# Kernel optimization log

Measured on AMD Instinct MI355X. Metric: run time of the kernel, lower is better.

The kernel has to match this reference:

```python
import jax, jax.numpy as jnp
import numpy as np

B, N, F, FH, H = 8, 2048, 64, 64, 4
NEG_BIG = -1e10


def setup_inputs() -> dict:
    key = jax.random.key(0)
    k_x, k_a, k_w, k_as, k_an = jax.random.split(key, 5)
    X = jax.random.normal(k_x, (B, N, F), dtype=jnp.float32)
    A = (jax.random.uniform(k_a, (B, N, N)) < 0.1).astype(jnp.float32)
    A = jnp.maximum(A, jnp.eye(N, dtype=jnp.float32)[None])
    W = jax.random.normal(k_w, (H, F, FH), dtype=jnp.float32) * (1.0 / np.sqrt(F))
    b = jnp.zeros((H, FH), dtype=jnp.float32)
    a_self = jax.random.normal(k_as, (H, FH), dtype=jnp.float32) * (1.0 / np.sqrt(FH))
    a_neigh = jax.random.normal(k_an, (H, FH), dtype=jnp.float32) * (1.0 / np.sqrt(FH))
    return {"X": X, "A": A, "W": W, "b": b, "a_self": a_self, "a_neigh": a_neigh}


def reference(X, A, W, b, a_self, a_neigh):
    # per-head linear projection: [B,H,N,FH]
    feats = jnp.einsum("bnf,hfo->bhno", X, W)
    # additive attention logits: e_ij = leaky_relu(a_s.h_i + a_n.h_j)
    s_self = jnp.einsum("bhno,ho->bhn", feats, a_self)   # [B,H,N]
    s_neigh = jnp.einsum("bhno,ho->bhn", feats, a_neigh)  # [B,H,N]
    scores = s_self[:, :, :, None] + s_neigh[:, :, None, :]  # [B,H,N,N]
    scores = jax.nn.leaky_relu(scores, negative_slope=0.2)
    scores = scores + (1.0 - A)[:, None] * NEG_BIG  # adjacency mask
    attn = jax.nn.softmax(scores, axis=-1)
    # weighted aggregation + bias (dropouts are identity at inference)
    out = jnp.einsum("bhnm,bhmo->bhno", attn, feats) + b[None, :, None, :]
    # concat heads -> [B,N,H*FH], then activation
    Bd, Hd, Nd, Fd = out.shape
    out = jnp.transpose(out, (0, 2, 1, 3)).reshape(Bd, Nd, Hd * Fd)
    return jax.nn.relu(out)
```

## Files before the change

kernel.cpp:

```cpp
#include <hip/hip_runtime.h>
#include <hip/hip_bf16.h>
#include <stdint.h>

#define B_ 8
#define N_ 2048
#define F_ 64
#define FH_ 64
#define H_ 4
#define C_ (H_*FH_)
#define CHUNK 64
#define NCHUNK (N_/CHUNK)
#define LOG2E 1.44269504088896340736f

typedef short short8 __attribute__((ext_vector_type(8)));
typedef float f32x4 __attribute__((ext_vector_type(4)));

__device__ __forceinline__ short f2bf(float f) {
    __hip_bfloat16 h = __float2bfloat16(f);
    return __builtin_bit_cast(short, h);
}

__device__ __forceinline__ void async16(void* l, const void* g) {
    __builtin_amdgcn_global_load_lds((const __attribute__((address_space(1))) unsigned int*)g,
                                     (__attribute__((address_space(3))) unsigned int*)l, 16, 0, 0);
}

__global__ __launch_bounds__(256) void kf(const float* __restrict__ A,
                                          const float* __restrict__ X,
                                          const float* __restrict__ W,
                                          const float* __restrict__ a_self,
                                          const float* __restrict__ a_neigh,
                                          unsigned long long* __restrict__ Amask,
                                          __hip_bfloat16* __restrict__ featsT,
                                          float* __restrict__ ss,
                                          float* __restrict__ sn) {
    __shared__ float a_lds[2][FH_];
    __shared__ __hip_bfloat16 cw_lds[FH_ * 72];
    const int bx = blockIdx.x;
    const int tid = threadIdx.x;
    const int wave = tid >> 6, lane = tid & 63;

    if (bx >= 1024) {
        const int R = (bx - 1024) * 4 + wave;
        const float* arow = A + (size_t)R * N_;
        unsigned long long* mrow = Amask + (size_t)R * (N_ / 64);
#pragma unroll
        for (int i = 0; i < 8; ++i) {
            float a0 = arow[i * 256 + lane];
            float a1 = arow[i * 256 + 64 + lane];
            float a2 = arow[i * 256 + 128 + lane];
            float a3 = arow[i * 256 + 192 + lane];
            unsigned long long m0 = __ballot(a0 != 0.0f);
            unsigned long long m1 = __ballot(a1 != 0.0f);
            unsigned long long m2 = __ballot(a2 != 0.0f);
            unsigned long long m3 = __ballot(a3 != 0.0f);
            if (lane == 0) {
                mrow[i * 4 + 0] = m0; mrow[i * 4 + 1] = m1;
                mrow[i * 4 + 2] = m2; mrow[i * 4 + 3] = m3;
            }
        }
        return;
    }

    const int nb = bx & 31, h = (bx >> 5) & 3, b = bx >> 7;

    if (tid < 64)       a_lds[0][tid] = a_self[h * FH_ + tid];
    else if (tid < 128) a_lds[1][tid - 64] = a_neigh[h * FH_ + tid - 64];
    {
        int f = tid >> 2, o0 = (tid & 3) * 16;
        const float* wsrc = W + ((size_t)(h * F_ + f)) * FH_ + o0;
#pragma unroll
        for (int k = 0; k < 16; ++k)
            cw_lds[(o0 + k) * 72 + f] = __float2bfloat16(wsrc[k]);
    }
    __syncthreads();

    const int m = lane & 15, q = lane >> 4;
    const int nl = wave * 16 + m;
    const int n = nb * 64 + nl;
    f32x4 acc[4] = {};
#pragma unroll
    for (int ks = 0; ks < 2; ++ks) {
        const float* xp = X + ((size_t)(b * N_ + n)) * F_ + ks * 32 + q * 8;
        float4 x0 = *(const float4*)xp;
        float4 x1 = *(const float4*)(xp + 4);
        short8 bfrag;
        bfrag[0] = f2bf(x0.x); bfrag[1] = f2bf(x0.y);
        bfrag[2] = f2bf(x0.z); bfrag[3] = f2bf(x0.w);
        bfrag[4] = f2bf(x1.x); bfrag[5] = f2bf(x1.y);
        bfrag[6] = f2bf(x1.z); bfrag[7] = f2bf(x1.w);
#pragma unroll
        for (int ot = 0; ot < 4; ++ot) {
            short8 afrag = *(const short8*)(cw_lds + (ot * 16 + m) * 72 + ks * 32 + q * 8);
            acc[ot] = __builtin_amdgcn_mfma_f32_16x16x32_bf16(afrag, bfrag, acc[ot], 0, 0, 0);
        }
    }
    __syncthreads();
    float ssv = 0.f, snv = 0.f;
#pragma unroll
    for (int ot = 0; ot < 4; ++ot) {
#pragma unroll
        for (int r = 0; r < 4; ++r) {
            int orow = ot * 16 + q * 4 + r;
            float v = acc[ot][r];
            cw_lds[orow * 72 + nl] = __float2bfloat16(v);
            ssv += v * a_lds[0][orow];
            snv += v * a_lds[1][orow];
        }
    }
    ssv += __shfl_xor(ssv, 16); ssv += __shfl_xor(ssv, 32);
    snv += __shfl_xor(snv, 16); snv += __shfl_xor(snv, 32);
    __syncthreads();
    {
        int o = tid >> 2, c = (tid & 3) * 16;
        const __hip_bfloat16* src = cw_lds + o * 72 + c;
        __hip_bfloat16* dst = featsT + ((size_t)(b * H_ + h) * FH_ + o) * N_ + nb * 64 + c;
        *(uint4*)dst       = *(const uint4*)src;
        *(uint4*)(dst + 8) = *(const uint4*)(src + 8);
    }
    if (lane < 16) {
        size_t idx = ((size_t)(b * H_ + h)) * N_ + n;
        ss[idx] = ssv * LOG2E;
        sn[idx] = snv * LOG2E;
    }
}

__global__ __launch_bounds__(256, 4) void k3_attn(const unsigned int* __restrict__ Amask,
                                                  const __hip_bfloat16* __restrict__ featsT,
                                                  const float* __restrict__ ss,
                                                  const float* __restrict__ sn,
                                                  const float* __restrict__ bias,
                                                  float* __restrict__ out) {
    __shared__ __hip_bfloat16 fv_lds[2][64 * CHUNK];
    __shared__ float e1_lds[N_];
    __shared__ float e2_lds[N_];

    const int L = blockIdx.x;
    const int g = L & 7;
    const int s = L >> 3;
    const int bh = g * 4 + (s >> 5);
    const int tile = s & 31;
    const int b = bh >> 2, h = bh & 3;

    const int tid = threadIdx.x, wave = tid >> 6, lane = tid & 63;
    const int m = lane & 15, q = lane >> 4;
    const int rowtile = tile * 64;

    {
        const float4* snrow = (const float4*)(sn + ((size_t)(b * H_ + h)) * N_);
        float4* e1v = (float4*)e1_lds;
        float4* e2v = (float4*)e2_lds;
#pragma unroll
        for (int i = 0; i < 2; ++i) {
            int idx = tid + i * 256;
            float4 v = snrow[idx];
            float4 u1, u2;
            u1.x = exp2f(v.x); u1.y = exp2f(v.y); u1.z = exp2f(v.z); u1.w = exp2f(v.w);
            u2.x = exp2f(0.2f * v.x); u2.y = exp2f(0.2f * v.y);
            u2.z = exp2f(0.2f * v.z); u2.w = exp2f(0.2f * v.w);
            e1v[idx] = u1; e2v[idx] = u2;
        }
    }
    const float ssi = ss[((size_t)(b * H_ + h)) * N_ + rowtile + wave * 16 + m];
    const float e1i = exp2f(ssi), e2i = exp2f(0.2f * ssi);

    const __hip_bfloat16* fhead = featsT + ((size_t)(b * H_ + h)) * FH_ * N_;
    const unsigned int* mrow = Amask + ((size_t)(b * N_) + rowtile + wave * 16 + m) * (N_ / 32);

    auto stage = [&](int c, int bufi) {
        const int cb = c * CHUNK;
#pragma unroll
        for (int i = 0; i < 2; ++i) {
            int base_unit = i * 256 + wave * 64;
            int unit = base_unit + lane;
            int o = unit >> 3, v = unit & 7;
            int u = v ^ (o & 7);
            async16(&fv_lds[bufi][base_unit * 8], fhead + (size_t)o * N_ + cb + u * 8);
        }
    };

    auto buildP = [&](int c, unsigned int mA, unsigned int mB, short8& pA, short8& pB) {
        const int cg = c * CHUNK;
        float4 eA10 = *(const float4*)(e1_lds + cg + q * 8);
        float4 eA11 = *(const float4*)(e1_lds + cg + q * 8 + 4);
        float4 eB10 = *(const float4*)(e1_lds + cg + 32 + q * 8);
        float4 eB11 = *(const float4*)(e1_lds + cg + 32 + q * 8 + 4);
        float4 eA20 = *(const float4*)(e2_lds + cg + q * 8);
        float4 eA21 = *(const float4*)(e2_lds + cg + q * 8 + 4);
        float4 eB20 = *(const float4*)(e2_lds + cg + 32 + q * 8);
        float4 eB21 = *(const float4*)(e2_lds + cg + 32 + q * 8 + 4);
        float e1A[8] = {eA10.x, eA10.y, eA10.z, eA10.w, eA11.x, eA11.y, eA11.z, eA11.w};
        float e1B[8] = {eB10.x, eB10.y, eB10.z, eB10.w, eB11.x, eB11.y, eB11.z, eB11.w};
        float e2A[8] = {eA20.x, eA20.y, eA20.z, eA20.w, eA21.x, eA21.y, eA21.z, eA21.w};
        float e2B[8] = {eB20.x, eB20.y, eB20.z, eB20.w, eB21.x, eB21.y, eB21.z, eB21.w};
#pragma unroll
        for (int t = 0; t < 8; ++t) {
            float vA = fmaxf(e1i * e1A[t], e2i * e2A[t]);
            float vB = fmaxf(e1i * e1B[t], e2i * e2B[t]);
            const int bit = q * 8 + t;
            pA[t] = (mA >> bit) & 1 ? f2bf(vA) : (short)0;
            pB[t] = (mB >> bit) & 1 ? f2bf(vB) : (short)0;
        }
    };

    uint2 mk_use = *(const uint2*)(mrow + 0);
    uint2 mk_a   = *(const uint2*)(mrow + 2);

    stage(0, 0);
    __syncthreads();

    f32x4 acc[2][4] = {};
    f32x4 accl[2] = {};
    short8 ones;
#pragma unroll
    for (int t = 0; t < 8; ++t) ones[t] = (short)0x3F80;

    short8 pA, pB;
    buildP(0, mk_use.x, mk_use.y, pA, pB);

    for (int c = 0; c < NCHUNK; ++c) {
        const int cur = c & 1;
        if (c + 1 < NCHUNK) stage(c + 1, cur ^ 1);
        uint2 mk_b = mk_a;
        if (c + 2 < NCHUNK) mk_b = *(const uint2*)(mrow + (c + 2) * 2);

        short8 fA[4], fB[4];
#pragma unroll
        for (int ct = 0; ct < 4; ++ct) {
            int o = ct * 16 + m;
            fA[ct] = *(const short8*)(fv_lds[cur] + ((o << 3) + (q ^ (o & 7))) * 8);
            fB[ct] = *(const short8*)(fv_lds[cur] + ((o << 3) + ((4 + q) ^ (o & 7))) * 8);
        }
#pragma unroll
        for (int ct = 0; ct < 4; ++ct) {
            acc[0][ct] = __builtin_amdgcn_mfma_f32_16x16x32_bf16(pA, fA[ct], acc[0][ct], 0, 0, 0);
            acc[1][ct] = __builtin_amdgcn_mfma_f32_16x16x32_bf16(pB, fB[ct], acc[1][ct], 0, 0, 0);
        }
        accl[0] = __builtin_amdgcn_mfma_f32_16x16x32_bf16(pA, ones, accl[0], 0, 0, 0);
        accl[1] = __builtin_amdgcn_mfma_f32_16x16x32_bf16(pB, ones, accl[1], 0, 0, 0);

        if (c + 1 < NCHUNK) buildP(c + 1, mk_a.x, mk_a.y, pA, pB);
        mk_a = mk_b;

        __syncthreads();
    }

    float bc[4];
#pragma unroll
    for (int ct = 0; ct < 4; ++ct) bc[ct] = bias[h * FH_ + ct * 16 + m];

#pragma unroll
    for (int r = 0; r < 4; ++r) {
        float inv = 1.0f / (accl[0][r] + accl[1][r]);
        int gr = rowtile + wave * 16 + q * 4 + r;
#pragma unroll
        for (int ct = 0; ct < 4; ++ct) {
            float v = (acc[0][ct][r] + acc[1][ct][r]) * inv + bc[ct];
            out[((size_t)(b * N_) + gr) * C_ + h * FH_ + ct * 16 + m] = fmaxf(v, 0.0f);
        }
    }
}

extern "C" void kernel_launch(void* const* d_in, const int* in_sizes, int n_in,
                              void* d_out, int out_size, void* d_ws, size_t ws_size,
                              hipStream_t stream) {
    const float* X       = (const float*)d_in[0];
    const float* A       = (const float*)d_in[1];
    const float* W       = (const float*)d_in[2];
    const float* bias    = (const float*)d_in[3];
    const float* a_self  = (const float*)d_in[4];
    const float* a_neigh = (const float*)d_in[5];
    float* out = (float*)d_out;

    char* ws = (char*)d_ws;
    __hip_bfloat16* featsT = (__hip_bfloat16*)(ws);
    float* ss              = (float*)(ws + 8421376);
    float* sn              = (float*)(ws + 8683520);
    unsigned long long* Am = (unsigned long long*)(ws + 8945664);

    kf      <<<5120, 256, 0, stream>>>(A, X, W, a_self, a_neigh, Am, featsT, ss, sn);
    k3_attn <<<1024, 256, 0, stream>>>((const unsigned int*)Am, featsT, ss, sn, bias, out);
}
```

Before: 250.4 us.

## Split attention columns across waves with per-wave staging and cross-wave reduction

Each wave now covers all 64 rows of the tile but only its own 512-column slice of neighbours. It stages its own feature chunk into a private LDS buffer, which removes the block-wide __syncthreads in the main loop and replaces them with per-wave waitcnt fences. Partial accumulators and row sums are combined through an LDS tree reduction at the end. The cost is more registers (launch bounds lowered from 4 to 2 blocks), reduction overhead, and an extra stall where each wave waits on its own async load with no double buffering.

```diff
diff --git a/kernel.cpp b/kernel.cpp
--- a/kernel.cpp
+++ b/kernel.cpp
@@ -9,7 +9,6 @@
 #define H_ 4
 #define C_ (H_*FH_)
 #define CHUNK 64
-#define NCHUNK (N_/CHUNK)
 #define LOG2E 1.44269504088896340736f
 
 typedef short short8 __attribute__((ext_vector_type(8)));
@@ -125,26 +124,24 @@
     }
 }
 
-__global__ __launch_bounds__(256, 4) void k3_attn(const unsigned int* __restrict__ Amask,
+__global__ __launch_bounds__(256, 2) void k3_attn(const unsigned int* __restrict__ Amask,
                                                   const __hip_bfloat16* __restrict__ featsT,
                                                   const float* __restrict__ ss,
                                                   const float* __restrict__ sn,
                                                   const float* __restrict__ bias,
                                                   float* __restrict__ out) {
-    __shared__ __hip_bfloat16 fv_lds[2][64 * CHUNK];
-    __shared__ float e1_lds[N_];
-    __shared__ float e2_lds[N_];
-
-    const int L = blockIdx.x;
-    const int g = L & 7;
-    const int s = L >> 3;
-    const int bh = g * 4 + (s >> 5);
-    const int tile = s & 31;
-    const int b = bh >> 2, h = bh & 3;
-
+    __shared__ char smem[49152];
+    float* e1_lds = (float*)smem;
+    float* e2_lds = (float*)(smem + 8192);
+    __hip_bfloat16* fv_all = (__hip_bfloat16*)(smem + 16384);
+
+    const int bx = blockIdx.x;
+    const int tile = bx & 31, h = (bx >> 5) & 3, b = bx >> 7;
     const int tid = threadIdx.x, wave = tid >> 6, lane = tid & 63;
     const int m = lane & 15, q = lane >> 4;
     const int rowtile = tile * 64;
+    const int colbase = wave * 512;
+    __hip_bfloat16* fvw = fv_all + wave * 4096;
 
     {
         const float4* snrow = (const float4*)(sn + ((size_t)(b * H_ + h)) * N_);
@@ -161,102 +158,152 @@
             e1v[idx] = u1; e2v[idx] = u2;
         }
     }
-    const float ssi = ss[((size_t)(b * H_ + h)) * N_ + rowtile + wave * 16 + m];
-    const float e1i = exp2f(ssi), e2i = exp2f(0.2f * ssi);
+    const float* ssrow = ss + ((size_t)(b * H_ + h)) * N_ + rowtile;
+    float e1i[4], e2i[4];
+#pragma unroll
+    for (int rg = 0; rg < 4; ++rg) {
+        float s_ = ssrow[rg * 16 + m];
+        e1i[rg] = exp2f(s_); e2i[rg] = exp2f(0.2f * s_);
+    }
 
     const __hip_bfloat16* fhead = featsT + ((size_t)(b * H_ + h)) * FH_ * N_;
-    const unsigned int* mrow = Amask + ((size_t)(b * N_) + rowtile + wave * 16 + m) * (N_ / 32);
-
-    auto stage = [&](int c, int bufi) {
-        const int cb = c * CHUNK;
-#pragma unroll
-        for (int i = 0; i < 2; ++i) {
-            int base_unit = i * 256 + wave * 64;
-            int unit = base_unit + lane;
+    const unsigned int* mrow = Amask + ((size_t)(b * N_) + rowtile + m) * (N_ / 32) + (colbase >> 5);
+
+    auto stage = [&](int c) {
+        const int cb = colbase + c * CHUNK;
+#pragma unroll
+        for (int i = 0; i < 8; ++i) {
+            int unit = i * 64 + lane;
             int o = unit >> 3, v = unit & 7;
             int u = v ^ (o & 7);
-            async16(&fv_lds[bufi][base_unit * 8], fhead + (size_t)o * N_ + cb + u * 8);
+            async16(fvw + (size_t)(i * 64) * 8, fhead + (size_t)o * N_ + cb + u * 8);
         }
     };
 
-    auto buildP = [&](int c, unsigned int mA, unsigned int mB, short8& pA, short8& pB) {
-        const int cg = c * CHUNK;
-        float4 eA10 = *(const float4*)(e1_lds + cg + q * 8);
-        float4 eA11 = *(const float4*)(e1_lds + cg + q * 8 + 4);
-        float4 eB10 = *(const float4*)(e1_lds + cg + 32 + q * 8);
-        float4 eB11 = *(const float4*)(e1_lds + cg + 32 + q * 8 + 4);
-        float4 eA20 = *(const float4*)(e2_lds + cg + q * 8);
-        float4 eA21 = *(const float4*)(e2_lds + cg + q * 8 + 4);
-        float4 eB20 = *(const float4*)(e2_lds + cg + 32 + q * 8);
-        float4 eB21 = *(const float4*)(e2_lds + cg + 32 + q * 8 + 4);
-        float e1A[8] = {eA10.x, eA10.y, eA10.z, eA10.w, eA11.x, eA11.y, eA11.z, eA11.w};
-        float e1B[8] = {eB10.x, eB10.y, eB10.z, eB10.w, eB11.x, eB11.y, eB11.z, eB11.w};
-        float e2A[8] = {eA20.x, eA20.y, eA20.z, eA20.w, eA21.x, eA21.y, eA21.z, eA21.w};
-        float e2B[8] = {eB20.x, eB20.y, eB20.z, eB20.w, eB21.x, eB21.y, eB21.z, eB21.w};
-#pragma unroll
-        for (int t = 0; t < 8; ++t) {
-            float vA = fmaxf(e1i * e1A[t], e2i * e2A[t]);
-            float vB = fmaxf(e1i * e1B[t], e2i * e2B[t]);
-            const int bit = q * 8 + t;
-            pA[t] = (mA >> bit) & 1 ? f2bf(vA) : (short)0;
-            pB[t] = (mB >> bit) & 1 ? f2bf(vB) : (short)0;
-        }
-    };
-
-    uint2 mk_use = *(const uint2*)(mrow + 0);
-    uint2 mk_a   = *(const uint2*)(mrow + 2);
-
-    stage(0, 0);
-    __syncthreads();
-
-    f32x4 acc[2][4] = {};
-    f32x4 accl[2] = {};
+    uint2 mk[4];
+#pragma unroll
+    for (int rg = 0; rg < 4; ++rg) mk[rg] = *(const uint2*)(mrow + rg * 1024);
+    stage(0);
+    __syncthreads();
+
+    f32x4 acc[4][4] = {};
+    f32x4 accl[4] = {};
     short8 ones;
 #pragma unroll
     for (int t = 0; t < 8; ++t) ones[t] = (short)0x3F80;
 
-    short8 pA, pB;
-    buildP(0, mk_use.x, mk_use.y, pA, pB);
-
-    for (int c = 0; c < NCHUNK; ++c) {
-        const int cur = c & 1;
-        if (c + 1 < NCHUNK) stage(c + 1, cur ^ 1);
-        uint2 mk_b = mk_a;
-        if (c + 2 < NCHUNK) mk_b = *(const uint2*)(mrow + (c + 2) * 2);
-
+    for (int c = 0; c < 8; ++c) {
         short8 fA[4], fB[4];
 #pragma unroll
         for (int ct = 0; ct < 4; ++ct) {
             int o = ct * 16 + m;
-            fA[ct] = *(const short8*)(fv_lds[cur] + ((o << 3) + (q ^ (o & 7))) * 8);
-            fB[ct] = *(const short8*)(fv_lds[cur] + ((o << 3) + ((4 + q) ^ (o & 7))) * 8);
-        }
-#pragma unroll
-        for (int ct = 0; ct < 4; ++ct) {
-            acc[0][ct] = __builtin_amdgcn_mfma_f32_16x16x32_bf16(pA, fA[ct], acc[0][ct], 0, 0, 0);
-            acc[1][ct] = __builtin_amdgcn_mfma_f32_16x16x32_bf16(pB, fB[ct], acc[1][ct], 0, 0, 0);
-        }
-        accl[0] = __builtin_amdgcn_mfma_f32_16x16x32_bf16(pA, ones, accl[0], 0, 0, 0);
-        accl[1] = __builtin_amdgcn_mfma_f32_16x16x32_bf16(pB, ones, accl[1], 0, 0, 0);
-
-        if (c + 1 < NCHUNK) buildP(c + 1, mk_a.x, mk_a.y, pA, pB);
-        mk_a = mk_b;
-
-        __syncthreads();
-    }
-
-    float bc[4];
-#pragma unroll
-    for (int ct = 0; ct < 4; ++ct) bc[ct] = bias[h * FH_ + ct * 16 + m];
-
-#pragma unroll
-    for (int r = 0; r < 4; ++r) {
-        float inv = 1.0f / (accl[0][r] + accl[1][r]);
-        int gr = rowtile + wave * 16 + q * 4 + r;
-#pragma unroll
-        for (int ct = 0; ct < 4; ++ct) {
-            float v = (acc[0][ct][r] + acc[1][ct][r]) * inv + bc[ct];
-            out[((size_t)(b * N_) + gr) * C_ + h * FH_ + ct * 16 + m] = fmaxf(v, 0.0f);
+            fA[ct] = *(const short8*)(fvw + ((o << 3) + (q ^ (o & 7))) * 8);
+            fB[ct] = *(const short8*)(fvw + ((o << 3) + ((4 + q) ^ (o & 7))) * 8);
+        }
+        asm volatile("s_waitcnt lgkmcnt(0)" ::: "memory");
+        __builtin_amdgcn_sched_barrier(0);
+        if (c + 1 < 8) stage(c + 1);
+        uint2 mkn[4];
+        if (c + 1 < 8) {
+#pragma unroll
+            for (int rg = 0; rg < 4; ++rg) mkn[rg] = *(const uint2*)(mrow + rg * 1024 + (c + 1) * 2);
+        }
+
+        const int cb = colbase + c * CHUNK;
+        float4 a10 = *(const float4*)(e1_lds + cb + q * 8);
+        float4 a11 = *(const float4*)(e1_lds + cb + q * 8 + 4);
+        float4 b10 = *(const float4*)(e1_lds + cb + 32 + q * 8);
+        float4 b11 = *(const float4*)(e1_lds + cb + 32 + q * 8 + 4);
+        float4 a20 = *(const float4*)(e2_lds + cb + q * 8);
+        float4 a21 = *(const float4*)(e2_lds + cb + q * 8 + 4);
+        float4 b20 = *(const float4*)(e2_lds + cb + 32 + q * 8);
+        float4 b21 = *(const float4*)(e2_lds + cb + 32 + q * 8 + 4);
+        float e1A[8] = {a10.x, a10.y, a10.z, a10.w, a11.x, a11.y, a11.z, a11.w};
+        float e1B[8] = {b10.x, b10.y, b10.z, b10.w, b11.x, b11.y, b11.z, b11.w};
+        float e2A[8] = {a20.x, a20.y, a20.z, a20.w, a21.x, a21.y, a21.z, a21.w};
+        float e2B[8] = {b20.x, b20.y, b20.z, b20.w, b21.x, b21.y, b21.z, b21.w};
+
+#pragma unroll
+        for (int rg = 0; rg < 4; ++rg) {
+            short8 pA, pB;
+            unsigned int mA = mk[rg].x, mB = mk[rg].y;
+#pragma unroll
+            for (int t = 0; t < 8; ++t) {
+                float vA = fmaxf(e1i[rg] * e1A[t], e2i[rg] * e2A[t]);
+                float vB = fmaxf(e1i[rg] * e1B[t], e2i[rg] * e2B[t]);
+                const int bit = q * 8 + t;
+                pA[t] = (mA >> bit) & 1 ? f2bf(vA) : (short)0;
+                pB[t] = (mB >> bit) & 1 ? f2bf(vB) : (short)0;
+            }
+#pragma unroll
+            for (int ct = 0; ct < 4; ++ct) {
+                acc[rg][ct] = __builtin_amdgcn_mfma_f32_16x16x32_bf16(pA, fA[ct], acc[rg][ct], 0, 0, 0);
+                acc[rg][ct] = __builtin_amdgcn_mfma_f32_16x16x32_bf16(pB, fB[ct], acc[rg][ct], 0, 0, 0);
+            }
+            accl[rg] = __builtin_amdgcn_mfma_f32_16x16x32_bf16(pA, ones, accl[rg], 0, 0, 0);
+            accl[rg] = __builtin_amdgcn_mfma_f32_16x16x32_bf16(pB, ones, accl[rg], 0, 0, 0);
+        }
+
+        if (c + 1 < 8) {
+            asm volatile("s_waitcnt vmcnt(0)" ::: "memory");
+            __builtin_amdgcn_sched_barrier(0);
+#pragma unroll
+            for (int rg = 0; rg < 4; ++rg) mk[rg] = mkn[rg];
+        }
+    }
+
+    float* red = (float*)(smem + 8192);
+    __syncthreads();
+    if (wave >= 2) {
+        float* base = red + (wave - 2) * 5120 + lane * 80;
+#pragma unroll
+        for (int rg = 0; rg < 4; ++rg) {
+#pragma unroll
+            for (int ct = 0; ct < 4; ++ct) *(f32x4*)(base + (rg * 4 + ct) * 4) = acc[rg][ct];
+            *(f32x4*)(base + 64 + rg * 4) = accl[rg];
+        }
+    }
+    __syncthreads();
+    if (wave < 2) {
+        const float* base = red + wave * 5120 + lane * 80;
+#pragma unroll
+        for (int rg = 0; rg < 4; ++rg) {
+#pragma unroll
+            for (int ct = 0; ct < 4; ++ct) acc[rg][ct] += *(const f32x4*)(base + (rg * 4 + ct) * 4);
+            accl[rg] += *(const f32x4*)(base + 64 + rg * 4);
+        }
+    }
+    __syncthreads();
+    if (wave == 1) {
+        float* base = red + lane * 80;
+#pragma unroll
+        for (int rg = 0; rg < 4; ++rg) {
+#pragma unroll
+            for (int ct = 0; ct < 4; ++ct) *(f32x4*)(base + (rg * 4 + ct) * 4) = acc[rg][ct];
+            *(f32x4*)(base + 64 + rg * 4) = accl[rg];
+        }
+    }
+    __syncthreads();
+    if (wave == 0) {
+        const float* base = red + lane * 80;
+        float bc[4];
+#pragma unroll
+        for (int ct = 0; ct < 4; ++ct) bc[ct] = bias[h * FH_ + ct * 16 + m];
+#pragma unroll
+        for (int rg = 0; rg < 4; ++rg) {
+#pragma unroll
+            for (int ct = 0; ct < 4; ++ct) acc[rg][ct] += *(const f32x4*)(base + (rg * 4 + ct) * 4);
+            accl[rg] += *(const f32x4*)(base + 64 + rg * 4);
+#pragma unroll
+            for (int r = 0; r < 4; ++r) {
+                float inv = 1.0f / accl[rg][r];
+                int gr = rowtile + rg * 16 + q * 4 + r;
+#pragma unroll
+                for (int ct = 0; ct < 4; ++ct) {
+                    float v = acc[rg][ct][r] * inv + bc[ct];
+                    out[((size_t)(b * N_) + gr) * C_ + h * FH_ + ct * 16 + m] = fmaxf(v, 0.0f);
+                }
+            }
         }
     }
 }
```

Measured after the change: 258.6 us. 1.03x slower.
